# Kernel optimization log

Measured on AMD Instinct MI355X. Metric: run time of the kernel, lower is better.

Reference implementation:

```python
import jax, jax.numpy as jnp
import numpy as np


def setup_inputs() -> dict:
    key = jax.random.key(0)
    k1, k2 = jax.random.split(key)
    tensor_1 = jax.random.normal(k1, (8192, 256), dtype=jnp.float32)
    tensor_2 = jax.random.normal(k2, (16384, 256), dtype=jnp.float32)
    return {"tensor_1": tensor_1, "tensor_2": tensor_2}


def reference(tensor_1, tensor_2):
    # L2-normalize along the feature dim (matches torch .norm(dim=-1), no eps)
    n1 = tensor_1 / jnp.linalg.norm(tensor_1, axis=-1, keepdims=True)  # [N, d]
    n2 = tensor_2 / jnp.linalg.norm(tensor_2, axis=-1, keepdims=True)  # [M, d]
    cos_sim = jnp.einsum("nd,md->nm", n1, n2)  # [N, M] cosine similarity
    top3, _ = jax.lax.top_k(cos_sim, 3)        # [N, 3]
    return top3.mean(axis=-1)                  # [N]
```

## Files before the change

### kernel.cpp

```cpp
#include <hip/hip_runtime.h>
#include <hip/hip_bf16.h>
#include <stdint.h>

#define N1 8192
#define N2 16384
#define DIM 256
#define BM 128
#define CS 8
#define COLS (N2 / CS)
#define TC 64
#define NT (COLS / TC)
#define NPART CS

typedef short v8s  __attribute__((ext_vector_type(8)));
typedef float f32x4 __attribute__((ext_vector_type(4)));

#define GLD16(g, l)                                                                         \
  __builtin_amdgcn_global_load_lds((const __attribute__((address_space(1))) uint32_t*)(g),  \
                                   (__attribute__((address_space(3))) uint32_t*)(l), 16, 0, 0)

__device__ __forceinline__ void top3_insert(float v, float& t0, float& t1, float& t2) {
    float nt1 = __builtin_amdgcn_fmed3f(v, t0, t1);
    float nt2 = __builtin_amdgcn_fmed3f(v, t1, t2);
    t0 = fmaxf(t0, v);
    t1 = nt1;
    t2 = nt2;
}

__global__ __launch_bounds__(256) void normalize_kernel(
        const float* __restrict__ inA, const float* __restrict__ inB,
        __hip_bfloat16* __restrict__ outA, __hip_bfloat16* __restrict__ outB) {
    const int wave = threadIdx.x >> 6;
    const int lane = threadIdx.x & 63;
    const int rgrp = lane >> 4;
    const int li   = lane & 15;
    const int gr   = blockIdx.x * 16 + wave * 4 + rgrp;
    const float* in;
    __hip_bfloat16* out;
    int row;
    if (gr < N1) { in = inA; out = outA; row = gr; }
    else         { in = inB; out = outB; row = gr - N1; }
    const float* rp = in + (size_t)row * DIM + li * 4;
    float4 v[4];
    #pragma unroll
    for (int j = 0; j < 4; ++j) v[j] = *(const float4*)(rp + j * 64);
    float s = 0.f;
    #pragma unroll
    for (int j = 0; j < 4; ++j)
        s += v[j].x * v[j].x + v[j].y * v[j].y + v[j].z * v[j].z + v[j].w * v[j].w;
    #pragma unroll
    for (int off = 8; off; off >>= 1) s += __shfl_xor(s, off, 64);
    const float inv = 1.0f / sqrtf(s);
    __hip_bfloat16* wp = out + (size_t)row * DIM + li * 4;
    #pragma unroll
    for (int j = 0; j < 4; ++j) {
        __hip_bfloat16 o[4];
        o[0] = __float2bfloat16(v[j].x * inv);
        o[1] = __float2bfloat16(v[j].y * inv);
        o[2] = __float2bfloat16(v[j].z * inv);
        o[3] = __float2bfloat16(v[j].w * inv);
        *(uint2*)(wp + j * 64) = *(uint2*)o;
    }
}

__global__ __launch_bounds__(256, 2) void gemm_top3_kernel(
        const __hip_bfloat16* __restrict__ A, const __hip_bfloat16* __restrict__ B,
        float* __restrict__ partial) {
    __shared__ char smem[2 * 32768];

    const int tid  = threadIdx.x;
    const int wave = tid >> 6;
    const int lane = tid & 63;
    const int lo   = lane & 15;
    const int quad = lane >> 4;
    const int cs   = blockIdx.x & 7;
    const int rb   = blockIdx.x >> 3;
    const int row0 = rb * BM;

    v8s af[2][8];
    {
        const char* arow = (const char*)A + (size_t)(row0 + wave * 32 + lo) * 512 + quad * 16;
        #pragma unroll
        for (int rt = 0; rt < 2; ++rt)
            #pragma unroll
            for (int s = 0; s < 8; ++s)
                af[rt][s] = *(const v8s*)(arow + rt * 8192 + s * 64);
    }
    asm volatile("s_waitcnt vmcnt(0)" ::: "memory");

    const char* Bb = (const char*)B + (size_t)cs * COLS * 512;
    int gsrc[8];
    #pragma unroll
    for (int j = 0; j < 8; ++j) {
        const int col = j * 8 + wave * 2 + (lane >> 5);
        gsrc[j] = col * 512 + (((lane & 31) ^ (col & 7)) << 4);
    }

    int swz[8];
    #pragma unroll
    for (int s = 0; s < 8; ++s) swz[s] = (((s * 4 + quad) ^ (lo & 7)) << 4);
    int bco[4];
    #pragma unroll
    for (int ct = 0; ct < 4; ++ct) bco[ct] = (ct * 16 + lo) * 512;

    float t0[8], t1[8], t2[8];
    #pragma unroll
    for (int i = 0; i < 8; ++i) { t0[i] = -1e30f; t1[i] = -1e30f; t2[i] = -1e30f; }

    #pragma unroll
    for (int j = 0; j < 8; ++j)
        GLD16(Bb + gsrc[j], smem + j * 4096 + wave * 1024);
    #pragma unroll
    for (int j = 0; j < 8; ++j)
        GLD16(Bb + 32768 + gsrc[j], smem + 32768 + j * 4096 + wave * 1024);

    #define DO_TILE(BOFF, GATE8, stage_ok, src_off)                                        \
    {                                                                                      \
        if (GATE8) asm volatile("s_waitcnt vmcnt(8)" ::: "memory");                        \
        else       asm volatile("s_waitcnt vmcnt(0)" ::: "memory");                        \
        __builtin_amdgcn_s_barrier();                                                      \
        f32x4 acc[2][4];                                                                   \
        __builtin_amdgcn_s_setprio(1);                                                     \
        _Pragma("unroll")                                                                  \
        for (int s = 0; s < 8; ++s) {                                                      \
            _Pragma("unroll")                                                              \
            for (int ct = 0; ct < 4; ++ct) {                                               \
                v8s bf = *(const v8s*)(smem + (BOFF) + bco[ct] + swz[s]);                  \
                _Pragma("unroll")                                                          \
                for (int rt = 0; rt < 2; ++rt) {                                           \
                    if (s == 0)                                                            \
                        acc[rt][ct] = __builtin_amdgcn_mfma_f32_16x16x32_bf16(             \
                            af[rt][0], bf, (f32x4){0.f, 0.f, 0.f, 0.f}, 0, 0, 0);          \
                    else                                                                   \
                        acc[rt][ct] = __builtin_amdgcn_mfma_f32_16x16x32_bf16(             \
                            af[rt][s], bf, acc[rt][ct], 0, 0, 0);                          \
                }                                                                          \
            }                                                                              \
        }                                                                                  \
        __builtin_amdgcn_s_setprio(0);                                                     \
        __builtin_amdgcn_s_barrier();                                                      \
        if (stage_ok) {                                                                    \
            const char* src = Bb + (size_t)(src_off);                                      \
            _Pragma("unroll")                                                              \
            for (int j = 0; j < 8; ++j)                                                    \
                GLD16(src + gsrc[j], smem + (BOFF) + j * 4096 + wave * 1024);              \
        }                                                                                  \
        _Pragma("unroll")                                                                  \
        for (int rt = 0; rt < 2; ++rt)                                                     \
            _Pragma("unroll")                                                              \
            for (int r = 0; r < 4; ++r) {                                                  \
                const int sl = rt * 4 + r;                                                 \
                _Pragma("unroll")                                                          \
                for (int ct = 0; ct < 4; ++ct)                                             \
                    top3_insert(acc[rt][ct][r], t0[sl], t1[sl], t2[sl]);                   \
            }                                                                              \
    }

    for (int tt = 0; tt < NT / 2; ++tt) {
        const int te = 2 * tt;
        const bool st = (tt < NT / 2 - 1);
        DO_TILE(0,     true, st, (size_t)(te + 2) * 32768);
        DO_TILE(32768, st,   st, (size_t)(te + 3) * 32768);
    }
    #undef DO_TILE

    #pragma unroll
    for (int sl = 0; sl < 8; ++sl) {
        #pragma unroll
        for (int step = 1; step < 16; step <<= 1) {
            float b0 = __shfl_xor(t0[sl], step, 64);
            float b1 = __shfl_xor(t1[sl], step, 64);
            float b2 = __shfl_xor(t2[sl], step, 64);
            top3_insert(b0, t0[sl], t1[sl], t2[sl]);
            top3_insert(b1, t0[sl], t1[sl], t2[sl]);
            top3_insert(b2, t0[sl], t1[sl], t2[sl]);
        }
    }
    if (lo == 0) {
        #pragma unroll
        for (int rt = 0; rt < 2; ++rt)
            #pragma unroll
            for (int r = 0; r < 4; ++r) {
                const int row = row0 + wave * 32 + rt * 16 + quad * 4 + r;
                float* p = partial + ((size_t)row * NPART + cs) * 3;
                const int sl = rt * 4 + r;
                p[0] = t0[sl]; p[1] = t1[sl]; p[2] = t2[sl];
            }
    }
}

__global__ __launch_bounds__(256) void merge_kernel(
        const float* __restrict__ partial, float* __restrict__ out) {
    const int row = blockIdx.x * 256 + threadIdx.x;
    if (row >= N1) return;
    const float4* p = (const float4*)(partial + (size_t)row * NPART * 3);
    float t0 = -1e30f, t1 = -1e30f, t2 = -1e30f;
    #pragma unroll
    for (int i = 0; i < 6; ++i) {
        float4 v = p[i];
        top3_insert(v.x, t0, t1, t2);
        top3_insert(v.y, t0, t1, t2);
        top3_insert(v.z, t0, t1, t2);
        top3_insert(v.w, t0, t1, t2);
    }
    out[row] = (t0 + t1 + t2) * (1.0f / 3.0f);
}

extern "C" void kernel_launch(void* const* d_in, const int* in_sizes, int n_in,
                              void* d_out, int out_size, void* d_ws, size_t ws_size,
                              hipStream_t stream) {
    const float* tA = (const float*)d_in[0];
    const float* tB = (const float*)d_in[1];
    float* out = (float*)d_out;

    __hip_bfloat16* An = (__hip_bfloat16*)d_ws;
    __hip_bfloat16* Bn = An + (size_t)N1 * DIM;
    float* partial = (float*)(Bn + (size_t)N2 * DIM);

    normalize_kernel<<<(N1 + N2) / 16, 256, 0, stream>>>(tA, tB, An, Bn);
    gemm_top3_kernel<<<(N1 / BM) * CS, 256, 0, stream>>>(An, Bn, partial);
    merge_kernel<<<N1 / 256, 256, 0, stream>>>(partial, out);
}
```

Baseline: 144.9 us.

## Retile GEMM-top3 to 256-row blocks with A fragments held in AGPRs

```diff
diff --git a/kernel.cpp b/kernel.cpp
--- a/kernel.cpp
+++ b/kernel.cpp
@@ -5,10 +5,10 @@
 #define N1 8192
 #define N2 16384
 #define DIM 256
-#define BM 128
-#define CS 8
+#define BM 256
+#define CS 16
 #define COLS (N2 / CS)
-#define TC 64
+#define TC 32
 #define NT (COLS / TC)
 #define NPART CS
 
@@ -66,32 +66,34 @@
 __global__ __launch_bounds__(256, 2) void gemm_top3_kernel(
         const __hip_bfloat16* __restrict__ A, const __hip_bfloat16* __restrict__ B,
         float* __restrict__ partial) {
-    __shared__ char smem[2 * 32768];
+    __shared__ char smem[2 * 16384];
 
     const int tid  = threadIdx.x;
     const int wave = tid >> 6;
     const int lane = tid & 63;
     const int lo   = lane & 15;
     const int quad = lane >> 4;
-    const int cs   = blockIdx.x & 7;
-    const int rb   = blockIdx.x >> 3;
+    const int cs   = blockIdx.x & 15;
+    const int rb   = blockIdx.x >> 4;
     const int row0 = rb * BM;
 
-    v8s af[2][8];
+    v8s af[4][8];
     {
-        const char* arow = (const char*)A + (size_t)(row0 + wave * 32 + lo) * 512 + quad * 16;
+        const char* arow = (const char*)A + (size_t)(row0 + wave * 64 + lo) * 512 + quad * 16;
         #pragma unroll
-        for (int rt = 0; rt < 2; ++rt)
+        for (int rt = 0; rt < 4; ++rt)
             #pragma unroll
-            for (int s = 0; s < 8; ++s)
-                af[rt][s] = *(const v8s*)(arow + rt * 8192 + s * 64);
+            for (int s = 0; s < 8; ++s) {
+                v8s t = *(const v8s*)(arow + rt * 8192 + s * 64);
+                asm("" : "=a"(af[rt][s]) : "0"(t));
+            }
     }
     asm volatile("s_waitcnt vmcnt(0)" ::: "memory");
 
     const char* Bb = (const char*)B + (size_t)cs * COLS * 512;
-    int gsrc[8];
-    #pragma unroll
-    for (int j = 0; j < 8; ++j) {
+    int gsrc[4];
+    #pragma unroll
+    for (int j = 0; j < 4; ++j) {
         const int col = j * 8 + wave * 2 + (lane >> 5);
         gsrc[j] = col * 512 + (((lane & 31) ^ (col & 7)) << 4);
     }
@@ -99,42 +101,42 @@
     int swz[8];
     #pragma unroll
     for (int s = 0; s < 8; ++s) swz[s] = (((s * 4 + quad) ^ (lo & 7)) << 4);
-    int bco[4];
-    #pragma unroll
-    for (int ct = 0; ct < 4; ++ct) bco[ct] = (ct * 16 + lo) * 512;
-
-    float t0[8], t1[8], t2[8];
-    #pragma unroll
-    for (int i = 0; i < 8; ++i) { t0[i] = -1e30f; t1[i] = -1e30f; t2[i] = -1e30f; }
-
-    #pragma unroll
-    for (int j = 0; j < 8; ++j)
+    const int bco0 = lo * 512;
+    const int bco1 = (16 + lo) * 512;
+
+    float t0[16], t1[16], t2[16];
+    #pragma unroll
+    for (int i = 0; i < 16; ++i) { t0[i] = -1e30f; t1[i] = -1e30f; t2[i] = -1e30f; }
+
+    #pragma unroll
+    for (int j = 0; j < 4; ++j)
         GLD16(Bb + gsrc[j], smem + j * 4096 + wave * 1024);
     #pragma unroll
-    for (int j = 0; j < 8; ++j)
-        GLD16(Bb + 32768 + gsrc[j], smem + 32768 + j * 4096 + wave * 1024);
-
-    #define DO_TILE(BOFF, GATE8, stage_ok, src_off)                                        \
+    for (int j = 0; j < 4; ++j)
+        GLD16(Bb + 16384 + gsrc[j], smem + 16384 + j * 4096 + wave * 1024);
+
+    #define DO_TILE(BOFF, GATE4, stage_ok, src_off)                                        \
     {                                                                                      \
-        if (GATE8) asm volatile("s_waitcnt vmcnt(8)" ::: "memory");                        \
+        if (GATE4) asm volatile("s_waitcnt vmcnt(4)" ::: "memory");                        \
         else       asm volatile("s_waitcnt vmcnt(0)" ::: "memory");                        \
         __builtin_amdgcn_s_barrier();                                                      \
-        f32x4 acc[2][4];                                                                   \
+        f32x4 acc[4][2];                                                                   \
+        _Pragma("unroll")                                                                  \
+        for (int rt = 0; rt < 4; ++rt) {                                                   \
+            acc[rt][0] = (f32x4){0.f, 0.f, 0.f, 0.f};                                      \
+            acc[rt][1] = (f32x4){0.f, 0.f, 0.f, 0.f};                                      \
+        }                                                                                  \
         __builtin_amdgcn_s_setprio(1);                                                     \
         _Pragma("unroll")                                                                  \
         for (int s = 0; s < 8; ++s) {                                                      \
+            v8s bf0 = *(const v8s*)(smem + (BOFF) + bco0 + swz[s]);                        \
+            v8s bf1 = *(const v8s*)(smem + (BOFF) + bco1 + swz[s]);                        \
             _Pragma("unroll")                                                              \
-            for (int ct = 0; ct < 4; ++ct) {                                               \
-                v8s bf = *(const v8s*)(smem + (BOFF) + bco[ct] + swz[s]);                  \
-                _Pragma("unroll")                                                          \
-                for (int rt = 0; rt < 2; ++rt) {                                           \
-                    if (s == 0)                                                            \
-                        acc[rt][ct] = __builtin_amdgcn_mfma_f32_16x16x32_bf16(             \
-                            af[rt][0], bf, (f32x4){0.f, 0.f, 0.f, 0.f}, 0, 0, 0);          \
-                    else                                                                   \
-                        acc[rt][ct] = __builtin_amdgcn_mfma_f32_16x16x32_bf16(             \
-                            af[rt][s], bf, acc[rt][ct], 0, 0, 0);                          \
-                }                                                                          \
+            for (int rt = 0; rt < 4; ++rt) {                                               \
+                asm("v_mfma_f32_16x16x32_bf16 %0, %1, %2, %0"                              \
+                    : "+v"(acc[rt][0]) : "a"(af[rt][s]), "v"(bf0));                        \
+                asm("v_mfma_f32_16x16x32_bf16 %0, %1, %2, %0"                              \
+                    : "+v"(acc[rt][1]) : "a"(af[rt][s]), "v"(bf1));                        \
             }                                                                              \
         }                                                                                  \
         __builtin_amdgcn_s_setprio(0);                                                     \
@@ -142,30 +144,29 @@
         if (stage_ok) {                                                                    \
             const char* src = Bb + (size_t)(src_off);                                      \
             _Pragma("unroll")                                                              \
-            for (int j = 0; j < 8; ++j)                                                    \
+            for (int j = 0; j < 4; ++j)                                                    \
                 GLD16(src + gsrc[j], smem + (BOFF) + j * 4096 + wave * 1024);              \
         }                                                                                  \
         _Pragma("unroll")                                                                  \
-        for (int rt = 0; rt < 2; ++rt)                                                     \
+        for (int rt = 0; rt < 4; ++rt)                                                     \
             _Pragma("unroll")                                                              \
             for (int r = 0; r < 4; ++r) {                                                  \
                 const int sl = rt * 4 + r;                                                 \
-                _Pragma("unroll")                                                          \
-                for (int ct = 0; ct < 4; ++ct)                                             \
-                    top3_insert(acc[rt][ct][r], t0[sl], t1[sl], t2[sl]);                   \
+                top3_insert(acc[rt][0][r], t0[sl], t1[sl], t2[sl]);                        \
+                top3_insert(acc[rt][1][r], t0[sl], t1[sl], t2[sl]);                        \
             }                                                                              \
     }
 
     for (int tt = 0; tt < NT / 2; ++tt) {
         const int te = 2 * tt;
         const bool st = (tt < NT / 2 - 1);
-        DO_TILE(0,     true, st, (size_t)(te + 2) * 32768);
-        DO_TILE(32768, st,   st, (size_t)(te + 3) * 32768);
+        DO_TILE(0,     true, st, (size_t)(te + 2) * 16384);
+        DO_TILE(16384, st,   st, (size_t)(te + 3) * 16384);
     }
     #undef DO_TILE
 
     #pragma unroll
-    for (int sl = 0; sl < 8; ++sl) {
+    for (int sl = 0; sl < 16; ++sl) {
         #pragma unroll
         for (int step = 1; step < 16; step <<= 1) {
             float b0 = __shfl_xor(t0[sl], step, 64);
@@ -178,10 +179,10 @@
     }
     if (lo == 0) {
         #pragma unroll
-        for (int rt = 0; rt < 2; ++rt)
+        for (int rt = 0; rt < 4; ++rt)
             #pragma unroll
             for (int r = 0; r < 4; ++r) {
-                const int row = row0 + wave * 32 + rt * 16 + quad * 4 + r;
+                const int row = row0 + wave * 64 + rt * 16 + quad * 4 + r;
                 float* p = partial + ((size_t)row * NPART + cs) * 3;
                 const int sl = rt * 4 + r;
                 p[0] = t0[sl]; p[1] = t1[sl]; p[2] = t2[sl];
@@ -196,7 +197,7 @@
     const float4* p = (const float4*)(partial + (size_t)row * NPART * 3);
     float t0 = -1e30f, t1 = -1e30f, t2 = -1e30f;
     #pragma unroll
-    for (int i = 0; i < 6; ++i) {
+    for (int i = 0; i < 12; ++i) {
         float4 v = p[i];
         top3_insert(v.x, t0, t1, t2);
         top3_insert(v.y, t0, t1, t2);
```

After: 138.2 us. -4.6%, faster.
